# Optimization experiments

Measured on AMD Instinct MI355X. Metric: run time of the kernel, lower is better.

## Reference

```python
import jax, jax.numpy as jnp
import numpy as np


def setup_inputs() -> dict:
    key = jax.random.key(0)
    B, T = 16, 2048
    # encoding dim must be T + 1 (1 padding row + T signal rows)
    x = jax.random.normal(key, (B, T + 1, T), dtype=jnp.float32)
    return {"x": x}


def reference(x):
    # x: [B, D, T] with D == T + 1
    B, D, T = x.shape
    pad = x[:, 0, :]                 # [B, T]  (index_select dim=1, idx [0])
    sig = x[:, 1:T + 1, :]           # [B, T, T] (index_select dim=1, idx 1..T)
    # L1 norm over encoding dim (torch.norm(signal, dim=1, p=1))
    sig_norm = jnp.sum(jnp.abs(sig), axis=1)          # [B, T]
    # 2-way softmax over (pad, norm); first column == sigmoid(pad - norm)
    w = jax.nn.sigmoid(pad - sig_norm)                # [B, T]
    pad_weighted = (w * pad)[:, None, :]              # [B, 1, T]
    # NB: torch reshapes signal to [B*T, T] row-major, so the (1 - w) gate
    # indexed by flat row i = (b, d) multiplies along the *encoding* axis.
    sig_weighted = (1.0 - w)[:, :, None] * sig        # [B, T, T]
    return jnp.concatenate([pad_weighted, sig_weighted], axis=1)  # [B, T+1, T]
```

## Files before the change

kernel.cpp:

```cpp
#include <hip/hip_runtime.h>


#define TDIM 2048
#define BDIM 16
#define ROWS 32
#define NTHREADS 512
#define NBLK (BDIM * (TDIM / ROWS))

typedef float floatx4 __attribute__((ext_vector_type(4)));

__global__ __launch_bounds__(NTHREADS, 8) void colsum_kernel(const float* __restrict__ x,
                                                             float* __restrict__ ws) {
    const int k  = blockIdx.x;
    const int b  = k >> 6;
    const int r0 = (k & 63) * ROWS;
    const int t  = threadIdx.x;

    const size_t plane = (size_t)(TDIM + 1) * TDIM;
    const float* src = x + (size_t)b * plane + TDIM + (size_t)r0 * TDIM + 4 * t;

    float a0 = 0.f, a1 = 0.f, a2 = 0.f, a3 = 0.f;
    #pragma unroll 8
    for (int r = 0; r < ROWS; ++r) {
        const floatx4 v = *reinterpret_cast<const floatx4*>(src + (size_t)r * TDIM);
        a0 += fabsf(v.x); a1 += fabsf(v.y); a2 += fabsf(v.z); a3 += fabsf(v.w);
    }

    floatx4 p4; p4.x = a0; p4.y = a1; p4.z = a2; p4.w = a3;
    *reinterpret_cast<floatx4*>(ws + (size_t)k * TDIM + 4 * t) = p4;
}

__global__ __launch_bounds__(NTHREADS, 8) void scale_kernel(const float* __restrict__ x,
                                                            const float* __restrict__ ws,
                                                            float* __restrict__ out) {
    const int k  = NBLK - 1 - blockIdx.x;
    const int b  = k >> 6;
    const int r0 = (k & 63) * ROWS;
    const int t  = threadIdx.x;

    const size_t plane = (size_t)(TDIM + 1) * TDIM;
    const float* xb  = x   + (size_t)b * plane;
    float*       ob  = out + (size_t)b * plane;
    const float* sig = xb + TDIM;

    __shared__ float red[16][ROWS];
    __shared__ float lds_scale[ROWS];
    const int c  = t & 31;
    const int jg = t >> 5;
    float s = 0.f;
    #pragma unroll
    for (int j = 0; j < 4; ++j)
        s += ws[(size_t)(b * 64 + jg * 4 + j) * TDIM + r0 + c];
    red[jg][c] = s;
    __syncthreads();

    if (t < ROWS) {
        float tot = 0.f;
        #pragma unroll
        for (int j = 0; j < 16; ++j) tot += red[j][t];
        const float p = xb[r0 + t];
        const float w = 1.0f / (1.0f + expf(tot - p));
        ob[r0 + t]    = w * p;
        lds_scale[t]  = 1.0f - w;
    }
    __syncthreads();

    const float* srcb = sig + (size_t)r0 * TDIM;
    float*       dstb = ob + TDIM + (size_t)r0 * TDIM;
    #pragma unroll 4
    for (int r = 0; r < ROWS; ++r) {
        floatx4 v = *reinterpret_cast<const floatx4*>(srcb + (size_t)r * TDIM + 4 * t);
        const float sc = lds_scale[r];
        v.x *= sc; v.y *= sc; v.z *= sc; v.w *= sc;
        __builtin_nontemporal_store(v, reinterpret_cast<floatx4*>(dstb + (size_t)r * TDIM + 4 * t));
    }
}

extern "C" void kernel_launch(void* const* d_in, const int* in_sizes, int n_in,
                              void* d_out, int out_size, void* d_ws, size_t ws_size,
                              hipStream_t stream) {
    const float* x   = (const float*)d_in[0];
    float*       out = (float*)d_out;
    float*       ws  = (float*)d_ws;

    colsum_kernel<<<NBLK, NTHREADS, 0, stream>>>(x, ws);
    scale_kernel <<<NBLK, NTHREADS, 0, stream>>>(x, ws, out);
}
```

Before: 140.1 us.

## Fuse colsum and scale into one persistent cooperative kernel with grid sync

Replaces the two-kernel launch with one persistent cooperative kernel. Blocks grid-stride over chunks to compute partial column sums, hit a grid-wide barrier, then do the reduction and scaling pass. This removes the second kernel launch and inter-kernel gap. In exchange it adds a grid-sync cost, runs fewer resident blocks, and loses the reversed block order that let the second kernel reuse cached data. An occupancy query each call adds host overhead, and the old two-kernel path is kept as a fallback.

```diff
diff --git a/kernel.cpp b/kernel.cpp
--- a/kernel.cpp
+++ b/kernel.cpp
@@ -1,13 +1,79 @@
 #include <hip/hip_runtime.h>
+#include <hip/hip_cooperative_groups.h>
+
+namespace cg = cooperative_groups;
 
 
 #define TDIM 2048
 #define BDIM 16
 #define ROWS 32
 #define NTHREADS 512
-#define NBLK (BDIM * (TDIM / ROWS))
+#define NCHUNK (BDIM * (TDIM / ROWS))
 
 typedef float floatx4 __attribute__((ext_vector_type(4)));
+
+__global__ __launch_bounds__(NTHREADS, 8) void pb_coop(const float* __restrict__ x,
+                                                       float* __restrict__ ws,
+                                                       float* __restrict__ out,
+                                                       int nblk) {
+    const int t = threadIdx.x;
+    const size_t plane = (size_t)(TDIM + 1) * TDIM;
+
+    for (int c = blockIdx.x; c < NCHUNK; c += nblk) {
+        const int b  = c >> 6;
+        const int r0 = (c & 63) * ROWS;
+        const float* src = x + (size_t)b * plane + TDIM + (size_t)r0 * TDIM + 4 * t;
+        float a0 = 0.f, a1 = 0.f, a2 = 0.f, a3 = 0.f;
+        #pragma unroll 8
+        for (int r = 0; r < ROWS; ++r) {
+            const floatx4 v = *reinterpret_cast<const floatx4*>(src + (size_t)r * TDIM);
+            a0 += fabsf(v.x); a1 += fabsf(v.y); a2 += fabsf(v.z); a3 += fabsf(v.w);
+        }
+        floatx4 p4; p4.x = a0; p4.y = a1; p4.z = a2; p4.w = a3;
+        *reinterpret_cast<floatx4*>(ws + (size_t)c * TDIM + 4 * t) = p4;
+    }
+
+    cg::this_grid().sync();
+
+    __shared__ float red[16][ROWS];
+    __shared__ float lds_scale[ROWS];
+    const int cc = t & 31;
+    const int jg = t >> 5;
+    for (int c = blockIdx.x; c < NCHUNK; c += nblk) {
+        const int b  = c >> 6;
+        const int r0 = (c & 63) * ROWS;
+        const float* xb = x   + (size_t)b * plane;
+        float*       ob = out + (size_t)b * plane;
+
+        float s = 0.f;
+        #pragma unroll
+        for (int j = 0; j < 4; ++j)
+            s += ws[(size_t)(b * 64 + jg * 4 + j) * TDIM + r0 + cc];
+        red[jg][cc] = s;
+        __syncthreads();
+
+        if (t < ROWS) {
+            float tot = 0.f;
+            #pragma unroll
+            for (int j = 0; j < 16; ++j) tot += red[j][t];
+            const float p = xb[r0 + t];
+            const float w = 1.0f / (1.0f + expf(tot - p));
+            ob[r0 + t]    = w * p;
+            lds_scale[t]  = 1.0f - w;
+        }
+        __syncthreads();
+
+        const float* srcb = xb + TDIM + (size_t)r0 * TDIM;
+        float*       dstb = ob + TDIM + (size_t)r0 * TDIM;
+        #pragma unroll 4
+        for (int r = 0; r < ROWS; ++r) {
+            floatx4 v = *reinterpret_cast<const floatx4*>(srcb + (size_t)r * TDIM + 4 * t);
+            const float sc = lds_scale[r];
+            v.x *= sc; v.y *= sc; v.z *= sc; v.w *= sc;
+            __builtin_nontemporal_store(v, reinterpret_cast<floatx4*>(dstb + (size_t)r * TDIM + 4 * t));
+        }
+    }
+}
 
 __global__ __launch_bounds__(NTHREADS, 8) void colsum_kernel(const float* __restrict__ x,
                                                              float* __restrict__ ws) {
@@ -15,17 +81,14 @@
     const int b  = k >> 6;
     const int r0 = (k & 63) * ROWS;
     const int t  = threadIdx.x;
-
     const size_t plane = (size_t)(TDIM + 1) * TDIM;
     const float* src = x + (size_t)b * plane + TDIM + (size_t)r0 * TDIM + 4 * t;
-
     float a0 = 0.f, a1 = 0.f, a2 = 0.f, a3 = 0.f;
     #pragma unroll 8
     for (int r = 0; r < ROWS; ++r) {
         const floatx4 v = *reinterpret_cast<const floatx4*>(src + (size_t)r * TDIM);
         a0 += fabsf(v.x); a1 += fabsf(v.y); a2 += fabsf(v.z); a3 += fabsf(v.w);
     }
-
     floatx4 p4; p4.x = a0; p4.y = a1; p4.z = a2; p4.w = a3;
     *reinterpret_cast<floatx4*>(ws + (size_t)k * TDIM + 4 * t) = p4;
 }
@@ -33,25 +96,23 @@
 __global__ __launch_bounds__(NTHREADS, 8) void scale_kernel(const float* __restrict__ x,
                                                             const float* __restrict__ ws,
                                                             float* __restrict__ out) {
-    const int k  = NBLK - 1 - blockIdx.x;
+    const int k  = NCHUNK - 1 - blockIdx.x;
     const int b  = k >> 6;
     const int r0 = (k & 63) * ROWS;
     const int t  = threadIdx.x;
-
     const size_t plane = (size_t)(TDIM + 1) * TDIM;
     const float* xb  = x   + (size_t)b * plane;
     float*       ob  = out + (size_t)b * plane;
-    const float* sig = xb + TDIM;
 
     __shared__ float red[16][ROWS];
     __shared__ float lds_scale[ROWS];
-    const int c  = t & 31;
+    const int cc = t & 31;
     const int jg = t >> 5;
     float s = 0.f;
     #pragma unroll
     for (int j = 0; j < 4; ++j)
-        s += ws[(size_t)(b * 64 + jg * 4 + j) * TDIM + r0 + c];
-    red[jg][c] = s;
+        s += ws[(size_t)(b * 64 + jg * 4 + j) * TDIM + r0 + cc];
+    red[jg][cc] = s;
     __syncthreads();
 
     if (t < ROWS) {
@@ -65,7 +126,7 @@
     }
     __syncthreads();
 
-    const float* srcb = sig + (size_t)r0 * TDIM;
+    const float* srcb = xb + TDIM + (size_t)r0 * TDIM;
     float*       dstb = ob + TDIM + (size_t)r0 * TDIM;
     #pragma unroll 4
     for (int r = 0; r < ROWS; ++r) {
@@ -83,6 +144,20 @@
     float*       out = (float*)d_out;
     float*       ws  = (float*)d_ws;
 
-    colsum_kernel<<<NBLK, NTHREADS, 0, stream>>>(x, ws);
-    scale_kernel <<<NBLK, NTHREADS, 0, stream>>>(x, ws, out);
+    int maxPerCU = 0;
+    hipError_t qerr = hipOccupancyMaxActiveBlocksPerMultiprocessor(&maxPerCU, pb_coop,
+                                                                   NTHREADS, 0);
+    int nblk = (qerr == hipSuccess) ? maxPerCU * 256 : 0;
+    if (nblk > NCHUNK) nblk = NCHUNK;
+
+    hipError_t lerr = hipErrorUnknown;
+    if (nblk > 0) {
+        void* args[] = { (void*)&x, (void*)&ws, (void*)&out, (void*)&nblk };
+        lerr = hipLaunchCooperativeKernel(pb_coop, dim3(nblk), dim3(NTHREADS),
+                                          args, 0, stream);
+    }
+    if (lerr != hipSuccess) {
+        colsum_kernel<<<NCHUNK, NTHREADS, 0, stream>>>(x, ws);
+        scale_kernel <<<NCHUNK, NTHREADS, 0, stream>>>(x, ws, out);
+    }
 }
```

Measured after the change: 211.2 us. 1.51x slower.
